# Optimization experiments

Measured on AMD Instinct MI355X. Metric: run time of the kernel, lower is better.

## Reference

```python
import jax, jax.numpy as jnp
import numpy as np

EPS = 1e-05
DILATION = 1

def setup_inputs() -> dict:
    key = jax.random.key(0)
    k1, k2 = jax.random.split(key)
    B, T, D, K = 4, 4096, 2048, 4
    x = jax.random.normal(k1, (B, T, D), dtype=jnp.float32)
    norm_weight = jnp.ones((D,), dtype=jnp.float32)
    conv_weight = jax.random.normal(k2, (D, 1, K), dtype=jnp.float32) * (1.0 / np.sqrt(K))
    return {"x": x, "norm_weight": norm_weight, "conv_weight": conv_weight}

def reference(x, norm_weight, conv_weight):
    B, T, D = x.shape
    K = conv_weight.shape[-1]
    pad = (K - 1) * DILATION
    # RMSNorm over last dim
    ms = jnp.mean(jnp.square(x), axis=-1, keepdims=True)
    y = x * jax.lax.rsqrt(ms + EPS) * norm_weight
    # to channel-first [B, D, T]
    y = jnp.transpose(y, (0, 2, 1))
    # causal depthwise conv: left-pad (K-1)*dilation, valid conv == torch pad-both + slice[:T]
    y = jax.lax.conv_general_dilated(
        y, conv_weight,
        window_strides=(1,),
        padding=[(pad, 0)],
        rhs_dilation=(DILATION,),
        dimension_numbers=("NCH", "OIH", "NCH"),
        feature_group_count=D,
    )
    # SiLU then back to [B, T, D]
    y = y * jax.nn.sigmoid(y)
    return jnp.transpose(y, (0, 2, 1))
```

## Files before the change

kernel.cpp:

```cpp
#include <hip/hip_runtime.h>
#include <math.h>

#define D_DIM 2048
#define T_DIM 4096
#define TT    4
#define NT    512
#define NW    8
#define NROW  (TT + 3)
#define ROW_F D_DIM
#define AS1 __attribute__((address_space(1)))
#define AS3 __attribute__((address_space(3)))

typedef float vfloat4 __attribute__((ext_vector_type(4)));

__device__ __forceinline__ float silu(float v) {
    return v * __builtin_amdgcn_rcpf(1.f + __expf(-v));
}

__device__ __forceinline__ void nt_store4(float* p, float a, float b, float c, float d) {
    vfloat4 v = { a, b, c, d };
    __builtin_nontemporal_store(v, (vfloat4*)p);
}

__global__ __launch_bounds__(NT, 4) void fused_kernel(
    const float* __restrict__ x,
    const float* __restrict__ g,
    const float* __restrict__ w,
    float* __restrict__ out)
{
    const int b    = blockIdx.y;
    const int t0   = blockIdx.x * TT;
    const int tid  = threadIdx.x;
    const int d0   = tid * 4;
    const int lane = tid & 63;
    const int wid  = tid >> 6;

    __shared__ __align__(16) float rows[NROW * ROW_F];
    __shared__ __align__(16) float inv_s[NROW];

    const float* xb = x + (size_t)b * T_DIM * D_DIM;

#pragma unroll
    for (int r = 0; r < NROW; ++r) {
        const int t = t0 - 3 + r;
        float* ldst = rows + r * ROW_F + d0;
        if (t >= 0) {
            const float* gsrc = xb + (size_t)t * D_DIM + d0;
            __builtin_amdgcn_global_load_lds((const AS1 void*)gsrc,
                                             (AS3 void*)ldst, 16, 0, 0);
        } else {
            *(float4*)ldst = make_float4(0.f, 0.f, 0.f, 0.f);
        }
    }

    const float4 gv = *(const float4*)(g + d0);
    float wgt[4][4];
#pragma unroll
    for (int j = 0; j < 4; ++j) {
        float4 wv = *(const float4*)(w + (size_t)(d0 + j) * 4);
        wgt[j][0] = wv.x; wgt[j][1] = wv.y; wgt[j][2] = wv.z; wgt[j][3] = wv.w;
    }

    __syncthreads();

    if (wid < NROW) {
        const float* rp = rows + wid * ROW_F;
        float p = 0.f;
#pragma unroll
        for (int j = 0; j < 8; ++j) {
            float4 v = *(const float4*)(rp + (j * 64 + lane) * 4);
            p = fmaf(v.x, v.x, p); p = fmaf(v.y, v.y, p);
            p = fmaf(v.z, v.z, p); p = fmaf(v.w, v.w, p);
        }
#pragma unroll
        for (int off = 32; off > 0; off >>= 1) p += __shfl_down(p, off, 64);
        if (lane == 0)
            inv_s[wid] = rsqrtf(p * (1.0f / D_DIM) + 1e-5f);
    }
    __syncthreads();

    float inv[NROW];
#pragma unroll
    for (int r = 0; r < NROW; ++r) inv[r] = inv_s[r];

    float n[NROW][4];
#pragma unroll
    for (int r = 0; r < NROW; ++r) {
        float4 v = *(const float4*)(rows + r * ROW_F + d0);
        n[r][0] = v.x * inv[r] * gv.x;
        n[r][1] = v.y * inv[r] * gv.y;
        n[r][2] = v.z * inv[r] * gv.z;
        n[r][3] = v.w * inv[r] * gv.w;
    }

    float* ob = out + (size_t)b * T_DIM * D_DIM + d0;
#pragma unroll
    for (int i = 0; i < TT; ++i) {
        float o[4];
#pragma unroll
        for (int j = 0; j < 4; ++j) {
            const float v = wgt[j][0] * n[i][j]     + wgt[j][1] * n[i + 1][j] +
                            wgt[j][2] * n[i + 2][j] + wgt[j][3] * n[i + 3][j];
            o[j] = silu(v);
        }
        nt_store4(ob + (size_t)(t0 + i) * D_DIM, o[0], o[1], o[2], o[3]);
    }
}

extern "C" void kernel_launch(void* const* d_in, const int* in_sizes, int n_in,
                              void* d_out, int out_size, void* d_ws, size_t ws_size,
                              hipStream_t stream) {
    const float* x = (const float*)d_in[0];
    const float* g = (const float*)d_in[1];
    const float* w = (const float*)d_in[2];
    float* out = (float*)d_out;

    const int total = in_sizes[0];
    const int rows  = total / D_DIM;
    const int B     = rows / T_DIM;

    dim3 grid(T_DIM / TT, B);
    fused_kernel<<<grid, NT, 0, stream>>>(x, g, w, out);
}
```

Before: 231.9 us.

## Process 32-timestep strips with double-buffered LDS pipeline and sliding conv window

Each block now covers a strip of 32 timesteps in chunks of 4, loading chunks asynchronously into a double-buffered LDS area while computing the previous one. The three causal halo rows are kept in registers as a sliding window, so each input row is read only once per strip instead of nearly twice. This reduces redundant global reads and overlaps load latency with compute, at the cost of fewer blocks in the grid and manual waitcnt/barrier synchronisation that must match outstanding memory ops.

```diff
diff --git a/kernel.cpp b/kernel.cpp
--- a/kernel.cpp
+++ b/kernel.cpp
@@ -3,10 +3,11 @@
 
 #define D_DIM 2048
 #define T_DIM 4096
-#define TT    4
 #define NT    512
 #define NW    8
-#define NROW  (TT + 3)
+#define CH    4
+#define NCH   8
+#define STRIP (CH * NCH)
 #define ROW_F D_DIM
 #define AS1 __attribute__((address_space(1)))
 #define AS3 __attribute__((address_space(3)))
@@ -29,29 +30,18 @@
     float* __restrict__ out)
 {
     const int b    = blockIdx.y;
-    const int t0   = blockIdx.x * TT;
+    const int t0   = blockIdx.x * STRIP;
     const int tid  = threadIdx.x;
     const int d0   = tid * 4;
     const int lane = tid & 63;
     const int wid  = tid >> 6;
 
-    __shared__ __align__(16) float rows[NROW * ROW_F];
-    __shared__ __align__(16) float inv_s[NROW];
+    __shared__ __align__(16) float buf[2][CH * ROW_F];
+    __shared__ __align__(16) float hpart[3][NW];
+    __shared__ __align__(16) float part[CH][2];
 
-    const float* xb = x + (size_t)b * T_DIM * D_DIM;
-
-#pragma unroll
-    for (int r = 0; r < NROW; ++r) {
-        const int t = t0 - 3 + r;
-        float* ldst = rows + r * ROW_F + d0;
-        if (t >= 0) {
-            const float* gsrc = xb + (size_t)t * D_DIM + d0;
-            __builtin_amdgcn_global_load_lds((const AS1 void*)gsrc,
-                                             (AS3 void*)ldst, 16, 0, 0);
-        } else {
-            *(float4*)ldst = make_float4(0.f, 0.f, 0.f, 0.f);
-        }
-    }
+    const float* xb = x   + (size_t)b * T_DIM * D_DIM;
+    float*       ob = out + (size_t)b * T_DIM * D_DIM + d0;
 
     const float4 gv = *(const float4*)(g + d0);
     float wgt[4][4];
@@ -61,49 +51,114 @@
         wgt[j][0] = wv.x; wgt[j][1] = wv.y; wgt[j][2] = wv.z; wgt[j][3] = wv.w;
     }
 
-    __syncthreads();
-
-    if (wid < NROW) {
-        const float* rp = rows + wid * ROW_F;
-        float p = 0.f;
+    float4 hv[3];
 #pragma unroll
-        for (int j = 0; j < 8; ++j) {
-            float4 v = *(const float4*)(rp + (j * 64 + lane) * 4);
-            p = fmaf(v.x, v.x, p); p = fmaf(v.y, v.y, p);
-            p = fmaf(v.z, v.z, p); p = fmaf(v.w, v.w, p);
-        }
+    for (int r = 0; r < 3; ++r) {
+        const int t = t0 - 3 + r;
+        hv[r] = (t >= 0) ? *(const float4*)(xb + (size_t)t * D_DIM + d0)
+                         : make_float4(0.f, 0.f, 0.f, 0.f);
+    }
+#pragma unroll
+    for (int r = 0; r < 3; ++r) {
+        float p = hv[r].x*hv[r].x + hv[r].y*hv[r].y + hv[r].z*hv[r].z + hv[r].w*hv[r].w;
 #pragma unroll
         for (int off = 32; off > 0; off >>= 1) p += __shfl_down(p, off, 64);
-        if (lane == 0)
-            inv_s[wid] = rsqrtf(p * (1.0f / D_DIM) + 1e-5f);
+        if (lane == 0) hpart[r][wid] = p;
     }
     __syncthreads();
 
-    float inv[NROW];
+    float win[3][4];
 #pragma unroll
-    for (int r = 0; r < NROW; ++r) inv[r] = inv_s[r];
-
-    float n[NROW][4];
-#pragma unroll
-    for (int r = 0; r < NROW; ++r) {
-        float4 v = *(const float4*)(rows + r * ROW_F + d0);
-        n[r][0] = v.x * inv[r] * gv.x;
-        n[r][1] = v.y * inv[r] * gv.y;
-        n[r][2] = v.z * inv[r] * gv.z;
-        n[r][3] = v.w * inv[r] * gv.w;
+    for (int r = 0; r < 3; ++r) {
+        const float* sp = hpart[r];
+        const float s = sp[0]+sp[1]+sp[2]+sp[3]+sp[4]+sp[5]+sp[6]+sp[7];
+        const float inv = rsqrtf(s * (1.0f / D_DIM) + 1e-5f);
+        win[r][0] = hv[r].x * inv * gv.x;
+        win[r][1] = hv[r].y * inv * gv.y;
+        win[r][2] = hv[r].z * inv * gv.z;
+        win[r][3] = hv[r].w * inv * gv.w;
     }
 
-    float* ob = out + (size_t)b * T_DIM * D_DIM + d0;
 #pragma unroll
-    for (int i = 0; i < TT; ++i) {
-        float o[4];
+    for (int cc = 0; cc < 2; ++cc) {
 #pragma unroll
-        for (int j = 0; j < 4; ++j) {
-            const float v = wgt[j][0] * n[i][j]     + wgt[j][1] * n[i + 1][j] +
-                            wgt[j][2] * n[i + 2][j] + wgt[j][3] * n[i + 3][j];
-            o[j] = silu(v);
+        for (int r = 0; r < CH; ++r) {
+            const float* gsrc = xb + (size_t)(t0 + cc * CH + r) * D_DIM + d0;
+            float* ldst = &buf[cc][r * ROW_F + d0];
+            __builtin_amdgcn_global_load_lds((const AS1 void*)gsrc,
+                                             (AS3 void*)ldst, 16, 0, 0);
         }
-        nt_store4(ob + (size_t)(t0 + i) * D_DIM, o[0], o[1], o[2], o[3]);
+    }
+    asm volatile("s_waitcnt vmcnt(4)" ::: "memory");
+    __builtin_amdgcn_s_barrier();
+
+#pragma unroll
+    for (int c = 0; c < NCH; ++c) {
+        const float* bp = buf[c & 1];
+
+        {
+            const int r = wid & 3, h = wid >> 2;
+            const float4* rp = (const float4*)(bp + r * ROW_F) + h * 256 + lane;
+            float p = 0.f;
+#pragma unroll
+            for (int j = 0; j < 4; ++j) {
+                float4 v = rp[j * 64];
+                p = fmaf(v.x, v.x, p); p = fmaf(v.y, v.y, p);
+                p = fmaf(v.z, v.z, p); p = fmaf(v.w, v.w, p);
+            }
+#pragma unroll
+            for (int off = 32; off > 0; off >>= 1) p += __shfl_down(p, off, 64);
+            if (lane == 0) part[r][h] = p;
+        }
+        asm volatile("s_waitcnt lgkmcnt(0)" ::: "memory");
+        __builtin_amdgcn_s_barrier();
+
+        float inv[CH];
+#pragma unroll
+        for (int r = 0; r < CH; ++r)
+            inv[r] = rsqrtf((part[r][0] + part[r][1]) * (1.0f / D_DIM) + 1e-5f);
+
+        float n[CH][4];
+#pragma unroll
+        for (int r = 0; r < CH; ++r) {
+            float4 v = *(const float4*)(bp + r * ROW_F + d0);
+            n[r][0] = v.x * inv[r] * gv.x;
+            n[r][1] = v.y * inv[r] * gv.y;
+            n[r][2] = v.z * inv[r] * gv.z;
+            n[r][3] = v.w * inv[r] * gv.w;
+        }
+#pragma unroll
+        for (int i = 0; i < CH; ++i) {
+            float o[4];
+#pragma unroll
+            for (int j = 0; j < 4; ++j) {
+                const float v = wgt[j][0] * win[0][j] + wgt[j][1] * win[1][j] +
+                                wgt[j][2] * win[2][j] + wgt[j][3] * n[i][j];
+                o[j] = silu(v);
+            }
+            nt_store4(ob + (size_t)(t0 + c * CH + i) * D_DIM, o[0], o[1], o[2], o[3]);
+#pragma unroll
+            for (int j = 0; j < 4; ++j) {
+                win[0][j] = win[1][j]; win[1][j] = win[2][j]; win[2][j] = n[i][j];
+            }
+        }
+
+        __builtin_amdgcn_sched_barrier(0);
+        if (c <= NCH - 3) {
+            __builtin_amdgcn_s_barrier();
+#pragma unroll
+            for (int r = 0; r < CH; ++r) {
+                const float* gsrc = xb + (size_t)(t0 + (c + 2) * CH + r) * D_DIM + d0;
+                float* ldst = &buf[c & 1][r * ROW_F + d0];
+                __builtin_amdgcn_global_load_lds((const AS1 void*)gsrc,
+                                                 (AS3 void*)ldst, 16, 0, 0);
+            }
+            asm volatile("s_waitcnt vmcnt(8)" ::: "memory");
+            __builtin_amdgcn_s_barrier();
+        } else if (c == NCH - 2) {
+            asm volatile("s_waitcnt vmcnt(4)" ::: "memory");
+            __builtin_amdgcn_s_barrier();
+        }
     }
 }
 
@@ -119,6 +174,6 @@
     const int rows  = total / D_DIM;
     const int B     = rows / T_DIM;
 
-    dim3 grid(T_DIM / TT, B);
+    dim3 grid(T_DIM / STRIP, B);
     fused_kernel<<<grid, NT, 0, stream>>>(x, g, w, out);
 }
```

After: 241.9 us. 1.04x slower.

## Split RMSNorm statistics into a separate kernel and stream conv from registers

Applied to the files above, without the earlier changes.

The fused LDS-staged kernel is replaced by two kernels. The first computes per-row inverse RMS into the workspace. The second has each thread load an 11-row register window straight from global memory and slide a 3-row window to do the causal conv plus SiLU over 8 timesteps. This drops the large LDS buffer, the block barriers and the repeated per-block reductions of halo rows, which should raise occupancy and memory-level parallelism. The cost is an extra full read of x, an extra kernel launch, and more registers per thread.

```diff
diff --git a/kernel.cpp b/kernel.cpp
--- a/kernel.cpp
+++ b/kernel.cpp
@@ -3,13 +3,8 @@
 
 #define D_DIM 2048
 #define T_DIM 4096
-#define TT    4
-#define NT    512
-#define NW    8
-#define NROW  (TT + 3)
-#define ROW_F D_DIM
-#define AS1 __attribute__((address_space(1)))
-#define AS3 __attribute__((address_space(3)))
+#define EPSI  1e-5f
+#define RB    8
 
 typedef float vfloat4 __attribute__((ext_vector_type(4)));
 
@@ -22,36 +17,50 @@
     __builtin_nontemporal_store(v, (vfloat4*)p);
 }
 
-__global__ __launch_bounds__(NT, 4) void fused_kernel(
+
+__global__ __launch_bounds__(256, 8) void rms_kernel(
+    const float* __restrict__ x, float* __restrict__ invs)
+{
+    const int row  = blockIdx.x * 4 + (threadIdx.x >> 6);
+    const int lane = threadIdx.x & 63;
+    const float* rp = x + (size_t)row * D_DIM + lane * 4;
+
+    float4 v[8];
+#pragma unroll
+    for (int j = 0; j < 8; ++j)
+        v[j] = *(const float4*)(rp + j * 256);
+
+    float a0 = 0.f, a1 = 0.f, a2 = 0.f, a3 = 0.f;
+#pragma unroll
+    for (int j = 0; j < 8; ++j) {
+        a0 = fmaf(v[j].x, v[j].x, a0);
+        a1 = fmaf(v[j].y, v[j].y, a1);
+        a2 = fmaf(v[j].z, v[j].z, a2);
+        a3 = fmaf(v[j].w, v[j].w, a3);
+    }
+    float p = (a0 + a1) + (a2 + a3);
+#pragma unroll
+    for (int off = 32; off > 0; off >>= 1) p += __shfl_down(p, off, 64);
+    if (lane == 0)
+        invs[row] = rsqrtf(p * (1.0f / D_DIM) + EPSI);
+}
+
+__global__ __launch_bounds__(512, 4) void conv_kernel(
     const float* __restrict__ x,
+    const float* __restrict__ invs,
     const float* __restrict__ g,
     const float* __restrict__ w,
     float* __restrict__ out)
 {
-    const int b    = blockIdx.y;
-    const int t0   = blockIdx.x * TT;
-    const int tid  = threadIdx.x;
-    const int d0   = tid * 4;
-    const int lane = tid & 63;
-    const int wid  = tid >> 6;
+    const int col = threadIdx.x;
+    const int grp = blockIdx.x;
+    const int b   = grp >> 9;
+    const int t0  = (grp & 511) * RB;
+    const int d0  = col * 4;
 
-    __shared__ __align__(16) float rows[NROW * ROW_F];
-    __shared__ __align__(16) float inv_s[NROW];
-
-    const float* xb = x + (size_t)b * T_DIM * D_DIM;
-
-#pragma unroll
-    for (int r = 0; r < NROW; ++r) {
-        const int t = t0 - 3 + r;
-        float* ldst = rows + r * ROW_F + d0;
-        if (t >= 0) {
-            const float* gsrc = xb + (size_t)t * D_DIM + d0;
-            __builtin_amdgcn_global_load_lds((const AS1 void*)gsrc,
-                                             (AS3 void*)ldst, 16, 0, 0);
-        } else {
-            *(float4*)ldst = make_float4(0.f, 0.f, 0.f, 0.f);
-        }
-    }
+    const float* xb = x    + (size_t)b * T_DIM * D_DIM + d0;
+    const float* ib = invs + (size_t)b * T_DIM;
+    float*       ob = out  + (size_t)b * T_DIM * D_DIM + d0;
 
     const float4 gv = *(const float4*)(g + d0);
     float wgt[4][4];
@@ -61,49 +70,48 @@
         wgt[j][0] = wv.x; wgt[j][1] = wv.y; wgt[j][2] = wv.z; wgt[j][3] = wv.w;
     }
 
-    __syncthreads();
+    float4 xv[RB + 3];
+    float  iv[RB + 3];
+#pragma unroll
+    for (int r = 0; r < RB + 3; ++r) {
+        const int t = t0 - 3 + r;
+        if (t >= 0) {
+            xv[r] = *(const float4*)(xb + (size_t)t * D_DIM);
+            iv[r] = ib[t];
+        } else {
+            xv[r] = make_float4(0.f, 0.f, 0.f, 0.f);
+            iv[r] = 0.f;
+        }
+    }
+    __builtin_amdgcn_sched_barrier(0);
 
-    if (wid < NROW) {
-        const float* rp = rows + wid * ROW_F;
-        float p = 0.f;
+    float win[3][4];
 #pragma unroll
-        for (int j = 0; j < 8; ++j) {
-            float4 v = *(const float4*)(rp + (j * 64 + lane) * 4);
-            p = fmaf(v.x, v.x, p); p = fmaf(v.y, v.y, p);
-            p = fmaf(v.z, v.z, p); p = fmaf(v.w, v.w, p);
-        }
-#pragma unroll
-        for (int off = 32; off > 0; off >>= 1) p += __shfl_down(p, off, 64);
-        if (lane == 0)
-            inv_s[wid] = rsqrtf(p * (1.0f / D_DIM) + 1e-5f);
-    }
-    __syncthreads();
-
-    float inv[NROW];
-#pragma unroll
-    for (int r = 0; r < NROW; ++r) inv[r] = inv_s[r];
-
-    float n[NROW][4];
-#pragma unroll
-    for (int r = 0; r < NROW; ++r) {
-        float4 v = *(const float4*)(rows + r * ROW_F + d0);
-        n[r][0] = v.x * inv[r] * gv.x;
-        n[r][1] = v.y * inv[r] * gv.y;
-        n[r][2] = v.z * inv[r] * gv.z;
-        n[r][3] = v.w * inv[r] * gv.w;
+    for (int r = 0; r < 3; ++r) {
+        win[r][0] = xv[r].x * iv[r] * gv.x;
+        win[r][1] = xv[r].y * iv[r] * gv.y;
+        win[r][2] = xv[r].z * iv[r] * gv.z;
+        win[r][3] = xv[r].w * iv[r] * gv.w;
     }
 
-    float* ob = out + (size_t)b * T_DIM * D_DIM + d0;
 #pragma unroll
-    for (int i = 0; i < TT; ++i) {
+    for (int i = 0; i < RB; ++i) {
+        const float4 xc = xv[i + 3];
+        const float  ic = iv[i + 3];
+        const float y[4] = { xc.x * ic * gv.x, xc.y * ic * gv.y,
+                             xc.z * ic * gv.z, xc.w * ic * gv.w };
         float o[4];
 #pragma unroll
         for (int j = 0; j < 4; ++j) {
-            const float v = wgt[j][0] * n[i][j]     + wgt[j][1] * n[i + 1][j] +
-                            wgt[j][2] * n[i + 2][j] + wgt[j][3] * n[i + 3][j];
+            const float v = wgt[j][0] * win[0][j] + wgt[j][1] * win[1][j] +
+                            wgt[j][2] * win[2][j] + wgt[j][3] * y[j];
             o[j] = silu(v);
         }
         nt_store4(ob + (size_t)(t0 + i) * D_DIM, o[0], o[1], o[2], o[3]);
+#pragma unroll
+        for (int j = 0; j < 4; ++j) {
+            win[0][j] = win[1][j]; win[1][j] = win[2][j]; win[2][j] = y[j];
+        }
     }
 }
 
@@ -113,12 +121,12 @@
     const float* x = (const float*)d_in[0];
     const float* g = (const float*)d_in[1];
     const float* w = (const float*)d_in[2];
-    float* out = (float*)d_out;
+    float* out  = (float*)d_out;
+    float* invs = (float*)d_ws;
 
     const int total = in_sizes[0];
     const int rows  = total / D_DIM;
-    const int B     = rows / T_DIM;
 
-    dim3 grid(T_DIM / TT, B);
-    fused_kernel<<<grid, NT, 0, stream>>>(x, g, w, out);
+    rms_kernel<<<dim3(rows / 4), 256, 0, stream>>>(x, invs);
+    conv_kernel<<<dim3(rows / RB), 512, 0, stream>>>(x, invs, g, w, out);
 }
```

Result: slower. 254.4 us (+9.7%).

## Double time tile and load halo rows into registers with sliding window

Applied to the files above, without the earlier changes.

Each block now covers 8 timesteps instead of 4, which cuts the 3-row halo re-read overhead from 7/4 to 11/8 reads per output row. The halo rows go straight into registers and are reduced with wave shuffles plus a small shared partial array, so all 8 waves compute row norms for the LDS tile. The conv runs as a sliding register window, dropping the per-row normalized array. Shared memory per block stays about the same (8 rows against 7), though register pressure and per-block latency rise.

```diff
diff --git a/kernel.cpp b/kernel.cpp
--- a/kernel.cpp
+++ b/kernel.cpp
@@ -3,10 +3,9 @@
 
 #define D_DIM 2048
 #define T_DIM 4096
-#define TT    4
+#define TT    8
 #define NT    512
 #define NW    8
-#define NROW  (TT + 3)
 #define ROW_F D_DIM
 #define AS1 __attribute__((address_space(1)))
 #define AS3 __attribute__((address_space(3)))
@@ -35,22 +34,27 @@
     const int lane = tid & 63;
     const int wid  = tid >> 6;
 
-    __shared__ __align__(16) float rows[NROW * ROW_F];
-    __shared__ __align__(16) float inv_s[NROW];
+    __shared__ __align__(16) float buf[TT * ROW_F];
+    __shared__ __align__(16) float hpart[3][NW];
+    __shared__ __align__(16) float inv_s[TT];
 
-    const float* xb = x + (size_t)b * T_DIM * D_DIM;
+    const float* xb = x   + (size_t)b * T_DIM * D_DIM;
+    float*       ob = out + (size_t)b * T_DIM * D_DIM + d0;
+
+    float4 hv[3];
+#pragma unroll
+    for (int r = 0; r < 3; ++r) {
+        const int t = t0 - 3 + r;
+        hv[r] = (t >= 0) ? *(const float4*)(xb + (size_t)t * D_DIM + d0)
+                         : make_float4(0.f, 0.f, 0.f, 0.f);
+    }
 
 #pragma unroll
-    for (int r = 0; r < NROW; ++r) {
-        const int t = t0 - 3 + r;
-        float* ldst = rows + r * ROW_F + d0;
-        if (t >= 0) {
-            const float* gsrc = xb + (size_t)t * D_DIM + d0;
-            __builtin_amdgcn_global_load_lds((const AS1 void*)gsrc,
-                                             (AS3 void*)ldst, 16, 0, 0);
-        } else {
-            *(float4*)ldst = make_float4(0.f, 0.f, 0.f, 0.f);
-        }
+    for (int r = 0; r < TT; ++r) {
+        const float* gsrc = xb + (size_t)(t0 + r) * D_DIM + d0;
+        float* ldst = buf + r * ROW_F + d0;
+        __builtin_amdgcn_global_load_lds((const AS1 void*)gsrc,
+                                         (AS3 void*)ldst, 16, 0, 0);
     }
 
     const float4 gv = *(const float4*)(g + d0);
@@ -61,10 +65,19 @@
         wgt[j][0] = wv.x; wgt[j][1] = wv.y; wgt[j][2] = wv.z; wgt[j][3] = wv.w;
     }
 
+#pragma unroll
+    for (int r = 0; r < 3; ++r) {
+        float p = hv[r].x*hv[r].x + hv[r].y*hv[r].y
+                + hv[r].z*hv[r].z + hv[r].w*hv[r].w;
+#pragma unroll
+        for (int off = 32; off > 0; off >>= 1) p += __shfl_down(p, off, 64);
+        if (lane == 0) hpart[r][wid] = p;
+    }
+
     __syncthreads();
 
-    if (wid < NROW) {
-        const float* rp = rows + wid * ROW_F;
+    {
+        const float* rp = buf + wid * ROW_F;
         float p = 0.f;
 #pragma unroll
         for (int j = 0; j < 8; ++j) {
@@ -74,36 +87,40 @@
         }
 #pragma unroll
         for (int off = 32; off > 0; off >>= 1) p += __shfl_down(p, off, 64);
-        if (lane == 0)
-            inv_s[wid] = rsqrtf(p * (1.0f / D_DIM) + 1e-5f);
+        if (lane == 0) inv_s[wid] = rsqrtf(p * (1.0f / D_DIM) + 1e-5f);
     }
     __syncthreads();
 
-    float inv[NROW];
+    float win[3][4];
 #pragma unroll
-    for (int r = 0; r < NROW; ++r) inv[r] = inv_s[r];
-
-    float n[NROW][4];
-#pragma unroll
-    for (int r = 0; r < NROW; ++r) {
-        float4 v = *(const float4*)(rows + r * ROW_F + d0);
-        n[r][0] = v.x * inv[r] * gv.x;
-        n[r][1] = v.y * inv[r] * gv.y;
-        n[r][2] = v.z * inv[r] * gv.z;
-        n[r][3] = v.w * inv[r] * gv.w;
+    for (int r = 0; r < 3; ++r) {
+        const float* sp = hpart[r];
+        const float s = sp[0]+sp[1]+sp[2]+sp[3]+sp[4]+sp[5]+sp[6]+sp[7];
+        const float inv = rsqrtf(s * (1.0f / D_DIM) + 1e-5f);
+        win[r][0] = hv[r].x * inv * gv.x;
+        win[r][1] = hv[r].y * inv * gv.y;
+        win[r][2] = hv[r].z * inv * gv.z;
+        win[r][3] = hv[r].w * inv * gv.w;
     }
 
-    float* ob = out + (size_t)b * T_DIM * D_DIM + d0;
 #pragma unroll
     for (int i = 0; i < TT; ++i) {
+        const float inv = inv_s[i];
+        float4 v = *(const float4*)(buf + i * ROW_F + d0);
+        const float y[4] = { v.x * inv * gv.x, v.y * inv * gv.y,
+                             v.z * inv * gv.z, v.w * inv * gv.w };
         float o[4];
 #pragma unroll
         for (int j = 0; j < 4; ++j) {
-            const float v = wgt[j][0] * n[i][j]     + wgt[j][1] * n[i + 1][j] +
-                            wgt[j][2] * n[i + 2][j] + wgt[j][3] * n[i + 3][j];
-            o[j] = silu(v);
+            const float t = wgt[j][0] * win[0][j] + wgt[j][1] * win[1][j] +
+                            wgt[j][2] * win[2][j] + wgt[j][3] * y[j];
+            o[j] = silu(t);
         }
         nt_store4(ob + (size_t)(t0 + i) * D_DIM, o[0], o[1], o[2], o[3]);
+#pragma unroll
+        for (int j = 0; j < 4; ++j) {
+            win[0][j] = win[1][j]; win[1][j] = win[2][j]; win[2][j] = y[j];
+        }
     }
 }
 
```

After: 236.2 us. No clear change (+1.8%).
